# Performance work log

Measured on AMD Instinct MI355X. Metric: run time of the kernel, lower is better.

The kernel has to match this reference:

```python
import jax, jax.numpy as jnp
import numpy as np


def build_perm(total_channels, num_filters):
    """Replicates Net.permuted_new_perfect's nested slice-copies as one gather index."""
    ncpf = total_channels // num_filters
    tg = num_filters + ncpf * ((num_filters - 1) * num_filters) // 2
    perm = np.zeros(tg * ncpf, dtype=np.int32)
    count = 0
    for i in range(num_filters):
        for j in range(ncpf):
            if j == 0:
                for k in range(i, num_filters):
                    perm[count] = i * ncpf
                    perm[count + 1:count + ncpf] = np.arange(k * ncpf + 1, k * ncpf + ncpf)
                    count += ncpf
            else:
                for k in range(i + 1, num_filters):
                    perm[count + j] = i * ncpf + j
                    perm[count:count + j] = np.arange(k * ncpf, k * ncpf + j)
                    perm[count + j + 1:count + ncpf] = np.arange(k * ncpf + j + 1, k * ncpf + ncpf)
                    count += ncpf
    return jnp.asarray(perm)


PERM1 = build_perm(18, 6)    # 153 gathered channels, 51 groups of 3
PERM2 = build_perm(255, 5)   # 26265 gathered channels, 515 groups of 51


def dw_conv(x, w, b, groups):
    y = jax.lax.conv_general_dilated(
        x, w, window_strides=(1, 1), padding='VALID',
        dimension_numbers=('NCHW', 'OIHW', 'NCHW'),
        feature_group_count=groups)
    return y + b[None, :, None, None]


def maxpool2(x):
    return jax.lax.reduce_window(x, -jnp.inf, jax.lax.max,
                                 (1, 1, 2, 2), (1, 1, 2, 2), 'VALID')


def perm_groupconv(x, perm, w, b):
    # gather channels, then grouped 1x1 conv (each group: ncpf chans -> 1 chan)
    G, ncpf = w.shape
    B, _, H, W = x.shape
    xg = x[:, perm].reshape(B, G, ncpf, H, W)
    return jnp.einsum('bgchw,gc->bghw', xg, w) + b[None, :, None, None]


def setup_inputs() -> dict:
    key = jax.random.key(0)
    ks = jax.random.split(key, 17)
    s = 0.05
    return {
        'x': jax.random.normal(ks[0], (64, 3, 32, 32), jnp.float32),
        'dw1_w': jax.random.normal(ks[1], (18, 1, 5, 5), jnp.float32) * s,
        'dw1_b': jax.random.normal(ks[2], (18,), jnp.float32) * s,
        'pc1_w': jax.random.normal(ks[3], (51, 3), jnp.float32) * s,
        'pc1_b': jax.random.normal(ks[4], (51,), jnp.float32) * s,
        'dw2_w': jax.random.normal(ks[5], (255, 1, 5, 5), jnp.float32) * s,
        'dw2_b': jax.random.normal(ks[6], (255,), jnp.float32) * s,
        'pc2_w': jax.random.normal(ks[7], (515, 51), jnp.float32) * s,
        'pc2_b': jax.random.normal(ks[8], (515,), jnp.float32) * s,
        'oo_w': jax.random.normal(ks[9], (100, 515), jnp.float32) * s,
        'oo_b': jax.random.normal(ks[10], (100,), jnp.float32) * s,
        'fc1_w': jax.random.normal(ks[11], (120, 2500), jnp.float32) * s,
        'fc1_b': jax.random.normal(ks[12], (120,), jnp.float32) * s,
        'fc2_w': jax.random.normal(ks[13], (84, 120), jnp.float32) * s,
        'fc2_b': jax.random.normal(ks[14], (84,), jnp.float32) * s,
        'fc3_w': jax.random.normal(ks[15], (10, 84), jnp.float32) * s,
        'fc3_b': jax.random.normal(ks[16], (10,), jnp.float32) * s,
    }


def reference(x, dw1_w, dw1_b, pc1_w, pc1_b, dw2_w, dw2_b, pc2_w, pc2_b,
              oo_w, oo_b, fc1_w, fc1_b, fc2_w, fc2_b, fc3_w, fc3_b):
    h = dw_conv(x, dw1_w, dw1_b, groups=3)            # [B,18,28,28]
    h = perm_groupconv(h, PERM1, pc1_w, pc1_b)        # [B,51,28,28]
    h = maxpool2(jax.nn.relu(h))                      # [B,51,14,14]
    h = dw_conv(h, dw2_w, dw2_b, groups=51)           # [B,255,10,10]
    h = perm_groupconv(h, PERM2, pc2_w, pc2_b)        # [B,515,10,10]
    h = maxpool2(jax.nn.relu(h))                      # [B,515,5,5]
    h = jax.nn.relu(jnp.einsum('bchw,oc->bohw', h, oo_w) + oo_b[None, :, None, None])  # [B,100,5,5]
    h = h.reshape(h.shape[0], -1)                     # [B,2500]
    h = jax.nn.relu(h @ fc1_w.T + fc1_b)
    h = jax.nn.relu(h @ fc2_w.T + fc2_b)
    return h @ fc3_w.T + fc3_b                        # [B,10]
```

## Files before the change

### kernel.cpp

```cpp
#include <hip/hip_runtime.h>

static constexpr size_t OFF_XT = 0;
static constexpr size_t OFF_H1 = 786432;
static constexpr size_t OFF_H2 = 4399104;
static constexpr size_t OFF_H3 = 6958080;
static constexpr size_t OFF_H4 = 13486080;
static constexpr size_t OFF_H5 = 16782080;
static constexpr size_t OFF_H5B = OFF_H1;
static constexpr size_t OFF_H6 = 17422080;
static constexpr size_t OFF_H7 = 17452800;
static constexpr size_t OFF_M1 = 17474304;
static constexpr size_t OFF_M2 = 17475328;
static constexpr size_t OFF_W2 = 17484032;

struct Meta2 { int g; int special; float wj; int valid; };

__device__ inline void scan_ijk(int F, int ncpf, int g, int& oi, int& oj, int& ok) {
  int cnt = 0;
  for (int i = 0; i < F; ++i)
    for (int j = 0; j < ncpf; ++j) {
      int ks = (j == 0) ? i : i + 1;
      for (int k = ks; k < F; ++k) {
        if (cnt == g) { oi = i; oj = j; ok = k; return; }
        ++cnt;
      }
    }
  oi = 0; oj = 0; ok = 0;
}

__global__ void k0_setup(const float* __restrict__ x, const float* __restrict__ pc2_w,
                         float* ws) {
  int bx = blockIdx.x, tid = threadIdx.x;
  if (bx < 96) {
    __shared__ float t[64][33];
    int c = bx >> 5, y = bx & 31;
    for (int r = 0; r < 8; ++r) {
      int b = r * 8 + (tid >> 5), xx = tid & 31;
      t[b][xx] = x[((b * 3 + c) * 32 + y) * 32 + xx];
    }
    __syncthreads();
    float* xT = ws + OFF_XT / 4;
    for (int r = 0; r < 8; ++r) {
      int xx = r * 4 + (tid >> 6), b = tid & 63;
      xT[((c * 32 + y) * 32 + xx) * 64 + b] = t[b][xx];
    }
  } else if (bx == 96) {
    if (tid < 51) {
      int i, j, k; scan_ijk(6, 3, tid, i, j, k);
      int* src1 = (int*)((char*)ws + OFF_M1);
      for (int p = 0; p < 3; ++p)
        src1[tid * 4 + p] = (p == j) ? (i * 3 + j) : (k * 3 + p);
    }
  } else {
    int idx = (bx - 97) * 256 + tid;
    if (idx < 536 * 51) {
      int s = idx / 51, p = idx - s * 51;
      int k, base;
      if (s < 8)        { k = 0; base = 0; }
      else if (s < 64)  { k = 1; base = 8; }
      else if (s < 168) { k = 2; base = 64; }
      else if (s < 328) { k = 3; base = 168; }
      else              { k = 4; base = 328; }
      int id2 = s - base;
      int cnt = 51 * k + 1;
      Meta2* m2 = (Meta2*)((char*)ws + OFF_M2);
      float* W2 = (float*)((char*)ws + OFF_W2);
      if (id2 < cnt) {
        int i, j;
        if (id2 <= k) { i = id2; j = 0; }
        else { int t2 = id2 - (k + 1); i = t2 / 50; j = t2 - i * 50 + 1; }
        int off = 205 * i - 51 * ((i * (i - 1)) >> 1);
        int g = (j == 0) ? (off + (k - i))
                         : (off + (5 - i) + (j - 1) * (4 - i) + (k - i - 1));
        W2[s * 51 + p] = (p == j) ? 0.f : pc2_w[g * 51 + p];
        if (p == 0) {
          m2[s].g = g; m2[s].special = i * 51 + j;
          m2[s].wj = pc2_w[g * 51 + j]; m2[s].valid = 1;
        }
      } else {
        W2[s * 51 + p] = 0.f;
        if (p == 0) { m2[s].g = 0; m2[s].special = 0; m2[s].wj = 0.f; m2[s].valid = 0; }
      }
    }
  }
}

__global__ void k1_dw1(const float* __restrict__ w, const float* __restrict__ bias,
                       float* ws) {
  const float* xT = ws + OFF_XT / 4;
  float* h1 = ws + OFF_H1 / 4;
  int b = threadIdx.x;
  int pos = blockIdx.x * 4 + threadIdx.y;
  int o = blockIdx.y;
  int y = pos / 28, xo = pos % 28;
  int c = o / 6;
  float acc = bias[o];
  #pragma unroll
  for (int ky = 0; ky < 5; ++ky)
    #pragma unroll
    for (int kx = 0; kx < 5; ++kx)
      acc = fmaf(xT[((c * 32 + y + ky) * 32 + xo + kx) * 64 + b],
                 w[o * 25 + ky * 5 + kx], acc);
  h1[((o * 28 + y) * 28 + xo) * 64 + b] = acc;
}

__global__ void k2_pc1(const float* __restrict__ w, const float* __restrict__ bias,
                       float* ws) {
  const float* h1 = ws + OFF_H1 / 4;
  const int* src1 = (const int*)((const char*)ws + OFF_M1);
  float* h2 = ws + OFF_H2 / 4;
  int b = threadIdx.x;
  int pos = blockIdx.x * 4 + threadIdx.y;
  int g = blockIdx.y;
  int py = pos / 14, px = pos % 14;
  int s0 = src1[g * 4 + 0], s1 = src1[g * 4 + 1], s2 = src1[g * 4 + 2];
  float w0 = w[g * 3 + 0], w1 = w[g * 3 + 1], w2 = w[g * 3 + 2], bb = bias[g];
  float m = 0.f;
  #pragma unroll
  for (int dy = 0; dy < 2; ++dy)
    #pragma unroll
    for (int dx = 0; dx < 2; ++dx) {
      int y = py * 2 + dy, xx = px * 2 + dx;
      float a = bb;
      a = fmaf(h1[((s0 * 28 + y) * 28 + xx) * 64 + b], w0, a);
      a = fmaf(h1[((s1 * 28 + y) * 28 + xx) * 64 + b], w1, a);
      a = fmaf(h1[((s2 * 28 + y) * 28 + xx) * 64 + b], w2, a);
      m = fmaxf(m, a);
    }
  h2[((g * 14 + py) * 14 + px) * 64 + b] = m;
}

__global__ void k3_dw2(const float* __restrict__ w, const float* __restrict__ bias,
                       float* ws) {
  const float* h2 = ws + OFF_H2 / 4;
  float* h3 = ws + OFF_H3 / 4;
  int b = threadIdx.x;
  int pos = blockIdx.x * 4 + threadIdx.y;
  int o = blockIdx.y;
  int y = pos / 10, xo = pos % 10;
  int c = o / 5;
  float acc = bias[o];
  #pragma unroll
  for (int ky = 0; ky < 5; ++ky)
    #pragma unroll
    for (int kx = 0; kx < 5; ++kx)
      acc = fmaf(h2[((c * 14 + y + ky) * 14 + xo + kx) * 64 + b],
                 w[o * 25 + ky * 5 + kx], acc);
  int py = y >> 1, dy = y & 1, px = xo >> 1, dx = xo & 1;
  h3[((o * 25 + py * 5 + px) * 4 + dy * 2 + dx) * 64 + b] = acc;
}

__global__ void __launch_bounds__(64) k4_pc2(const float* __restrict__ bias, float* ws) {
  const float* h3 = ws + OFF_H3 / 4;
  const float* W2 = (const float*)((const char*)ws + OFF_W2);
  const Meta2* m2 = (const Meta2*)((const char*)ws + OFF_M2);
  float* h4 = ws + OFF_H4 / 4;
  int b = threadIdx.x;
  int pyx = blockIdx.x;
  int chunk = blockIdx.y;
  int k;
  if (chunk < 1) k = 0; else if (chunk < 8) k = 1; else if (chunk < 21) k = 2;
  else if (chunk < 41) k = 3; else k = 4;
  int s0 = chunk * 8;
  float acc[8][4];
  #pragma unroll
  for (int m = 0; m < 8; ++m)
    #pragma unroll
    for (int q = 0; q < 4; ++q) acc[m][q] = 0.f;
  const float* hb = h3 + (size_t)(k * 51 * 100 + pyx * 4) * 64 + b;
  for (int p = 0; p < 51; ++p) {
    float v0 = hb[p * 6400 + 0];
    float v1 = hb[p * 6400 + 64];
    float v2 = hb[p * 6400 + 128];
    float v3 = hb[p * 6400 + 192];
    #pragma unroll
    for (int m = 0; m < 8; ++m) {
      float wv = W2[(s0 + m) * 51 + p];
      acc[m][0] = fmaf(v0, wv, acc[m][0]);
      acc[m][1] = fmaf(v1, wv, acc[m][1]);
      acc[m][2] = fmaf(v2, wv, acc[m][2]);
      acc[m][3] = fmaf(v3, wv, acc[m][3]);
    }
  }
  #pragma unroll
  for (int m = 0; m < 8; ++m) {
    Meta2 mm = m2[s0 + m];
    if (!mm.valid) continue;
    const float* hs = h3 + (size_t)(mm.special * 100 + pyx * 4) * 64 + b;
    float bb = bias[mm.g];
    float r0 = fmaf(hs[0],   mm.wj, acc[m][0]) + bb;
    float r1 = fmaf(hs[64],  mm.wj, acc[m][1]) + bb;
    float r2 = fmaf(hs[128], mm.wj, acc[m][2]) + bb;
    float r3 = fmaf(hs[192], mm.wj, acc[m][3]) + bb;
    float r = fmaxf(fmaxf(r0, r1), fmaxf(r2, r3));
    h4[(mm.g * 25 + pyx) * 64 + b] = fmaxf(r, 0.f);
  }
}

__global__ void __launch_bounds__(256) k5_oo(const float* __restrict__ w, float* ws) {
  const float* h4 = ws + OFF_H4 / 4;
  __shared__ float red[4][4][64];
  int lane = threadIdx.x, wv = threadIdx.y;
  int pyx = blockIdx.x, og = blockIdx.y, ks = blockIdx.z;
  int kb = ks ? 258 : 0;
  int kn = ks ? 257 : 258;
  int q = kn >> 2, r = kn & 3;
  int base = kb + wv * q + (wv < r ? wv : r);
  int n = q + (wv < r ? 1 : 0);
  const float* w0 = w + (og * 4 + 0) * 515;
  const float* w1 = w + (og * 4 + 1) * 515;
  const float* w2 = w + (og * 4 + 2) * 515;
  const float* w3 = w + (og * 4 + 3) * 515;
  const float* hp = h4 + pyx * 64 + lane;
  float a0 = 0.f, a1 = 0.f, a2 = 0.f, a3 = 0.f;
  #pragma unroll 4
  for (int i = 0; i < n; ++i) {
    int c = base + i;
    float v = hp[c * 1600];
    a0 = fmaf(v, w0[c], a0);
    a1 = fmaf(v, w1[c], a1);
    a2 = fmaf(v, w2[c], a2);
    a3 = fmaf(v, w3[c], a3);
  }
  red[wv][0][lane] = a0; red[wv][1][lane] = a1;
  red[wv][2][lane] = a2; red[wv][3][lane] = a3;
  __syncthreads();
  if (wv == 0) {
    float* h5p = ws + (ks ? OFF_H5B : OFF_H5) / 4;
    #pragma unroll
    for (int m = 0; m < 4; ++m) {
      float s = red[0][m][lane] + red[1][m][lane] + red[2][m][lane] + red[3][m][lane];
      h5p[((og * 4 + m) * 25 + pyx) * 64 + lane] = s;
    }
  }
}

__global__ void __launch_bounds__(256) k6_fc1(const float* __restrict__ w,
                                              const float* __restrict__ oo_b, float* ws) {
  const float* h5a = ws + OFF_H5 / 4;
  const float* h5b = ws + OFF_H5B / 4;
  float* h6 = ws + OFF_H6 / 4;
  __shared__ float red[4][4][64];
  int lane = threadIdx.x, wv = threadIdx.y;
  int og = blockIdx.x, ks = blockIdx.y;
  int kb = ks * 312 + (ks < 4 ? ks : 4);
  int kn = 312 + (ks < 4 ? 1 : 0);
  int q = kn >> 2, r = kn & 3;
  int base = kb + wv * q + (wv < r ? wv : r);
  int n = q + (wv < r ? 1 : 0);
  const float* w0 = w + (og * 4 + 0) * 2500;
  const float* w1 = w + (og * 4 + 1) * 2500;
  const float* w2 = w + (og * 4 + 2) * 2500;
  const float* w3 = w + (og * 4 + 3) * 2500;
  float a0 = 0.f, a1 = 0.f, a2 = 0.f, a3 = 0.f;
  #pragma unroll 4
  for (int i = 0; i < n; ++i) {
    int k = base + i;
    float v = fmaxf(h5a[k * 64 + lane] + h5b[k * 64 + lane] + oo_b[k / 25], 0.f);
    a0 = fmaf(v, w0[k], a0);
    a1 = fmaf(v, w1[k], a1);
    a2 = fmaf(v, w2[k], a2);
    a3 = fmaf(v, w3[k], a3);
  }
  red[wv][0][lane] = a0; red[wv][1][lane] = a1;
  red[wv][2][lane] = a2; red[wv][3][lane] = a3;
  __syncthreads();
  if (wv == 0) {
    #pragma unroll
    for (int m = 0; m < 4; ++m) {
      float s = red[0][m][lane] + red[1][m][lane] + red[2][m][lane] + red[3][m][lane];
      atomicAdd(&h6[(og * 4 + m) * 64 + lane], s);
    }
  }
}

__global__ void __launch_bounds__(256) k7_fc2(const float* __restrict__ w,
                                              const float* __restrict__ fc1_b,
                                              const float* __restrict__ bias, float* ws) {
  const float* h6 = ws + OFF_H6 / 4;
  float* h7 = ws + OFF_H7 / 4;
  __shared__ float red[4][64];
  int lane = threadIdx.x & 63, wv = threadIdx.x >> 6;
  int o = blockIdx.x;
  float acc = 0.f;
  int i0 = wv * 30;
  #pragma unroll 5
  for (int i = i0; i < i0 + 30; ++i) {
    float v = fmaxf(h6[i * 64 + lane] + fc1_b[i], 0.f);
    acc = fmaf(v, w[o * 120 + i], acc);
  }
  red[wv][lane] = acc;
  __syncthreads();
  if (threadIdx.x < 64) {
    float s = red[0][lane] + red[1][lane] + red[2][lane] + red[3][lane] + bias[o];
    h7[o * 64 + lane] = fmaxf(s, 0.f);
  }
}

__global__ void __launch_bounds__(256) k8_fc3(const float* __restrict__ w,
                                              const float* __restrict__ bias,
                                              float* out, const float* ws) {
  const float* h7 = ws + OFF_H7 / 4;
  __shared__ float red[4][64];
  int lane = threadIdx.x & 63, wv = threadIdx.x >> 6;
  int o = blockIdx.x;
  float acc = 0.f;
  int i0 = wv * 21;
  #pragma unroll 7
  for (int i = i0; i < i0 + 21; ++i)
    acc = fmaf(h7[i * 64 + lane], w[o * 84 + i], acc);
  red[wv][lane] = acc;
  __syncthreads();
  if (threadIdx.x < 64) {
    float s = red[0][lane] + red[1][lane] + red[2][lane] + red[3][lane] + bias[o];
    out[lane * 10 + o] = s;
  }
}

extern "C" void kernel_launch(void* const* d_in, const int* in_sizes, int n_in,
                              void* d_out, int out_size, void* d_ws, size_t ws_size,
                              hipStream_t stream) {
  const float* x     = (const float*)d_in[0];
  const float* dw1_w = (const float*)d_in[1];
  const float* dw1_b = (const float*)d_in[2];
  const float* pc1_w = (const float*)d_in[3];
  const float* pc1_b = (const float*)d_in[4];
  const float* dw2_w = (const float*)d_in[5];
  const float* dw2_b = (const float*)d_in[6];
  const float* pc2_w = (const float*)d_in[7];
  const float* pc2_b = (const float*)d_in[8];
  const float* oo_w  = (const float*)d_in[9];
  const float* oo_b  = (const float*)d_in[10];
  const float* fc1_w = (const float*)d_in[11];
  const float* fc1_b = (const float*)d_in[12];
  const float* fc2_w = (const float*)d_in[13];
  const float* fc2_b = (const float*)d_in[14];
  const float* fc3_w = (const float*)d_in[15];
  const float* fc3_b = (const float*)d_in[16];
  float* ws = (float*)d_ws;
  float* out = (float*)d_out;

  hipMemsetAsync((char*)d_ws + OFF_H6, 0, 120 * 64 * 4, stream);

  hipLaunchKernelGGL(k0_setup, dim3(204), dim3(256), 0, stream, x, pc2_w, ws);
  hipLaunchKernelGGL(k1_dw1, dim3(196, 18), dim3(64, 4), 0, stream, dw1_w, dw1_b, ws);
  hipLaunchKernelGGL(k2_pc1, dim3(49, 51), dim3(64, 4), 0, stream, pc1_w, pc1_b, ws);
  hipLaunchKernelGGL(k3_dw2, dim3(25, 255), dim3(64, 4), 0, stream, dw2_w, dw2_b, ws);
  hipLaunchKernelGGL(k4_pc2, dim3(25, 67), dim3(64), 0, stream, pc2_b, ws);
  hipLaunchKernelGGL(k5_oo, dim3(25, 25, 2), dim3(64, 4), 0, stream, oo_w, ws);
  hipLaunchKernelGGL(k6_fc1, dim3(30, 8), dim3(64, 4), 0, stream, fc1_w, oo_b, ws);
  hipLaunchKernelGGL(k7_fc2, dim3(84), dim3(256), 0, stream, fc2_w, fc1_b, fc2_b, ws);
  hipLaunchKernelGGL(k8_fc3, dim3(10), dim3(256), 0, stream, fc3_w, fc3_b, out, ws);
}
```

Baseline: 171.7 us.

## Fuse fc2/fc3 into one tail kernel, fold memset into setup, split pc2 across waves

Three changes land together. The memset of the fc1 accumulator becomes extra blocks in the setup kernel, which removes one API call. The fc2 and fc3 kernels merge into a single one-block kernel that keeps activations in shared memory, which removes a launch and the global round trip for h7. k4_pc2 now uses 4 waves per block, each handling 2 output groups instead of 8 per wave, which raises parallelism and cuts register pressure but means each wave re-reads the h3 input.

```diff
diff --git a/kernel.cpp b/kernel.cpp
--- a/kernel.cpp
+++ b/kernel.cpp
@@ -8,7 +8,6 @@
 static constexpr size_t OFF_H5 = 16782080;
 static constexpr size_t OFF_H5B = OFF_H1;
 static constexpr size_t OFF_H6 = 17422080;
-static constexpr size_t OFF_H7 = 17452800;
 static constexpr size_t OFF_M1 = 17474304;
 static constexpr size_t OFF_M2 = 17475328;
 static constexpr size_t OFF_W2 = 17484032;
@@ -51,7 +50,7 @@
       for (int p = 0; p < 3; ++p)
         src1[tid * 4 + p] = (p == j) ? (i * 3 + j) : (k * 3 + p);
     }
-  } else {
+  } else if (bx < 204) {
     int idx = (bx - 97) * 256 + tid;
     if (idx < 536 * 51) {
       int s = idx / 51, p = idx - s * 51;
@@ -82,6 +81,9 @@
         if (p == 0) { m2[s].g = 0; m2[s].special = 0; m2[s].wj = 0.f; m2[s].valid = 0; }
       }
     }
+  } else {
+    int idx = (bx - 204) * 256 + tid;
+    if (idx < 7680) (ws + OFF_H6 / 4)[idx] = 0.f;
   }
 }
 
@@ -150,40 +152,43 @@
   h3[((o * 25 + py * 5 + px) * 4 + dy * 2 + dx) * 64 + b] = acc;
 }
 
-__global__ void __launch_bounds__(64) k4_pc2(const float* __restrict__ bias, float* ws) {
+__global__ void __launch_bounds__(256) k4_pc2(const float* __restrict__ bias, float* ws) {
   const float* h3 = ws + OFF_H3 / 4;
   const float* W2 = (const float*)((const char*)ws + OFF_W2);
   const Meta2* m2 = (const Meta2*)((const char*)ws + OFF_M2);
   float* h4 = ws + OFF_H4 / 4;
-  int b = threadIdx.x;
+  int b = threadIdx.x, wv = threadIdx.y;
   int pyx = blockIdx.x;
   int chunk = blockIdx.y;
   int k;
   if (chunk < 1) k = 0; else if (chunk < 8) k = 1; else if (chunk < 21) k = 2;
   else if (chunk < 41) k = 3; else k = 4;
-  int s0 = chunk * 8;
-  float acc[8][4];
-  #pragma unroll
-  for (int m = 0; m < 8; ++m)
+  int s0 = chunk * 8 + wv * 2;
+  float acc[2][4];
+  #pragma unroll
+  for (int m = 0; m < 2; ++m)
     #pragma unroll
     for (int q = 0; q < 4; ++q) acc[m][q] = 0.f;
   const float* hb = h3 + (size_t)(k * 51 * 100 + pyx * 4) * 64 + b;
+  const float* wr0 = W2 + (s0 + 0) * 51;
+  const float* wr1 = W2 + (s0 + 1) * 51;
   for (int p = 0; p < 51; ++p) {
     float v0 = hb[p * 6400 + 0];
     float v1 = hb[p * 6400 + 64];
     float v2 = hb[p * 6400 + 128];
     float v3 = hb[p * 6400 + 192];
-    #pragma unroll
-    for (int m = 0; m < 8; ++m) {
-      float wv = W2[(s0 + m) * 51 + p];
-      acc[m][0] = fmaf(v0, wv, acc[m][0]);
-      acc[m][1] = fmaf(v1, wv, acc[m][1]);
-      acc[m][2] = fmaf(v2, wv, acc[m][2]);
-      acc[m][3] = fmaf(v3, wv, acc[m][3]);
-    }
-  }
-  #pragma unroll
-  for (int m = 0; m < 8; ++m) {
+    float wa = wr0[p], wb = wr1[p];
+    acc[0][0] = fmaf(v0, wa, acc[0][0]);
+    acc[0][1] = fmaf(v1, wa, acc[0][1]);
+    acc[0][2] = fmaf(v2, wa, acc[0][2]);
+    acc[0][3] = fmaf(v3, wa, acc[0][3]);
+    acc[1][0] = fmaf(v0, wb, acc[1][0]);
+    acc[1][1] = fmaf(v1, wb, acc[1][1]);
+    acc[1][2] = fmaf(v2, wb, acc[1][2]);
+    acc[1][3] = fmaf(v3, wb, acc[1][3]);
+  }
+  #pragma unroll
+  for (int m = 0; m < 2; ++m) {
     Meta2 mm = m2[s0 + m];
     if (!mm.valid) continue;
     const float* hs = h3 + (size_t)(mm.special * 100 + pyx * 4) * 64 + b;
@@ -274,46 +279,37 @@
   }
 }
 
-__global__ void __launch_bounds__(256) k7_fc2(const float* __restrict__ w,
-                                              const float* __restrict__ fc1_b,
-                                              const float* __restrict__ bias, float* ws) {
+__global__ void __launch_bounds__(1024) k7_tail(const float* __restrict__ w2,
+                                                const float* __restrict__ fc1_b,
+                                                const float* __restrict__ b2,
+                                                const float* __restrict__ w3,
+                                                const float* __restrict__ b3,
+                                                float* out, const float* ws) {
   const float* h6 = ws + OFF_H6 / 4;
-  float* h7 = ws + OFF_H7 / 4;
-  __shared__ float red[4][64];
-  int lane = threadIdx.x & 63, wv = threadIdx.x >> 6;
-  int o = blockIdx.x;
-  float acc = 0.f;
-  int i0 = wv * 30;
-  #pragma unroll 5
-  for (int i = i0; i < i0 + 30; ++i) {
-    float v = fmaxf(h6[i * 64 + lane] + fc1_b[i], 0.f);
-    acc = fmaf(v, w[o * 120 + i], acc);
-  }
-  red[wv][lane] = acc;
+  __shared__ float a6[120][64];
+  __shared__ float a7[84][64];
+  int lane = threadIdx.x, wv = threadIdx.y;
+  int tid = wv * 64 + lane;
+  for (int idx = tid; idx < 120 * 64; idx += 1024) {
+    int i = idx >> 6, b = idx & 63;
+    a6[i][b] = fmaxf(h6[idx] + fc1_b[i], 0.f);
+  }
   __syncthreads();
-  if (threadIdx.x < 64) {
-    float s = red[0][lane] + red[1][lane] + red[2][lane] + red[3][lane] + bias[o];
-    h7[o * 64 + lane] = fmaxf(s, 0.f);
-  }
-}
-
-__global__ void __launch_bounds__(256) k8_fc3(const float* __restrict__ w,
-                                              const float* __restrict__ bias,
-                                              float* out, const float* ws) {
-  const float* h7 = ws + OFF_H7 / 4;
-  __shared__ float red[4][64];
-  int lane = threadIdx.x & 63, wv = threadIdx.x >> 6;
-  int o = blockIdx.x;
-  float acc = 0.f;
-  int i0 = wv * 21;
-  #pragma unroll 7
-  for (int i = i0; i < i0 + 21; ++i)
-    acc = fmaf(h7[i * 64 + lane], w[o * 84 + i], acc);
-  red[wv][lane] = acc;
+  for (int o = wv; o < 84; o += 16) {
+    float acc = b2[o];
+    #pragma unroll 8
+    for (int i = 0; i < 120; ++i)
+      acc = fmaf(a6[i][lane], w2[o * 120 + i], acc);
+    a7[o][lane] = fmaxf(acc, 0.f);
+  }
   __syncthreads();
-  if (threadIdx.x < 64) {
-    float s = red[0][lane] + red[1][lane] + red[2][lane] + red[3][lane] + bias[o];
-    out[lane * 10 + o] = s;
+  if (wv < 10) {
+    int o = wv;
+    float acc = b3[o];
+    #pragma unroll 12
+    for (int i = 0; i < 84; ++i)
+      acc = fmaf(a7[i][lane], w3[o * 84 + i], acc);
+    out[lane * 10 + o] = acc;
   }
 }
 
@@ -340,15 +336,13 @@
   float* ws = (float*)d_ws;
   float* out = (float*)d_out;
 
-  hipMemsetAsync((char*)d_ws + OFF_H6, 0, 120 * 64 * 4, stream);
-
-  hipLaunchKernelGGL(k0_setup, dim3(204), dim3(256), 0, stream, x, pc2_w, ws);
+  hipLaunchKernelGGL(k0_setup, dim3(234), dim3(256), 0, stream, x, pc2_w, ws);
   hipLaunchKernelGGL(k1_dw1, dim3(196, 18), dim3(64, 4), 0, stream, dw1_w, dw1_b, ws);
   hipLaunchKernelGGL(k2_pc1, dim3(49, 51), dim3(64, 4), 0, stream, pc1_w, pc1_b, ws);
   hipLaunchKernelGGL(k3_dw2, dim3(25, 255), dim3(64, 4), 0, stream, dw2_w, dw2_b, ws);
-  hipLaunchKernelGGL(k4_pc2, dim3(25, 67), dim3(64), 0, stream, pc2_b, ws);
+  hipLaunchKernelGGL(k4_pc2, dim3(25, 67), dim3(64, 4), 0, stream, pc2_b, ws);
   hipLaunchKernelGGL(k5_oo, dim3(25, 25, 2), dim3(64, 4), 0, stream, oo_w, ws);
   hipLaunchKernelGGL(k6_fc1, dim3(30, 8), dim3(64, 4), 0, stream, fc1_w, oo_b, ws);
-  hipLaunchKernelGGL(k7_fc2, dim3(84), dim3(256), 0, stream, fc2_w, fc1_b, fc2_b, ws);
-  hipLaunchKernelGGL(k8_fc3, dim3(10), dim3(256), 0, stream, fc3_w, fc3_b, out, ws);
-}
+  hipLaunchKernelGGL(k7_tail, dim3(1), dim3(64, 16), 0, stream,
+                     fc2_w, fc1_b, fc2_b, fc3_w, fc3_b, out, ws);
+}
```

New measurement: 191.7 us. 11.6% more time.
